# Performance work log

Measured on AMD Instinct MI355X. Metric: run time of the kernel, lower is better.

## Reference

```python
import jax, jax.numpy as jnp
import numpy as np

EPS = 1e-5

def _ln(z, g, b):
    # LayerNorm over last axis (per the gammas/betas of shape (2, 3H))
    mu = jnp.mean(z, axis=-1, keepdims=True)
    var = jnp.var(z, axis=-1, keepdims=True)
    return g * (z - mu) * jax.lax.rsqrt(var + EPS) + b

def setup_inputs() -> dict:
    key = jax.random.key(0)
    ks = jax.random.split(key, 12)
    B, L, D_IN, H, A, DEPTH = 64, 512, 256, 256, 128, 4
    glorot = lambda k, sh: jax.random.normal(k, sh, jnp.float32) * np.sqrt(2.0 / (sh[0] + sh[1])).astype(np.float32)
    # variable-length prefix masks (bucketing/masking semantics of the layer)
    lengths = jax.random.randint(ks[0], (B, 1), L // 2, L + 1)
    mask = jnp.arange(L)[None, :] < lengths
    return {
        'x': jax.random.normal(ks[1], (B, L, D_IN), jnp.float32),
        'mask': mask,
        'W_emb': glorot(ks[2], (D_IN, H)),
        'b_emb': jnp.zeros((H,), jnp.float32),
        'W': glorot(ks[3], (H, 3 * H)),
        'U': glorot(ks[4], (H, 3 * H)),
        'b': jnp.zeros((3 * H,), jnp.float32),
        'W_action_1': glorot(ks[5], (H, A)),
        'U_action_1': glorot(ks[6], (H, A)),
        'b_action_1': jnp.zeros((A,), jnp.float32),
        'W_action_2': glorot(ks[7], (A, 2)),
        'b_action_2': jnp.zeros((2,), jnp.float32),
        'gammas': jnp.ones((2, 3 * H), jnp.float32),
        'betas': jnp.zeros((2, 3 * H), jnp.float32),
        'depth': DEPTH,
    }

def _run_depth(x_seq, m_seq, W, U, b, Wa1, Ua1, ba1, Wa2, ba2, gammas, betas):
    # x_seq: (L,B,H), m_seq: (L,B) bool
    H = W.shape[0]
    B = x_seq.shape[1]
    # precompute + layernorm the input projection for all steps (fusable)
    xp_all = _ln(jnp.einsum('lbh,hk->lbk', x_seq, W), gammas[0], betas[0])  # (L,B,3H)

    def step(h, inputs):
        xp, xt, mt = inputs  # (B,3H), (B,H), (B,)
        hp = _ln(h @ U, gammas[1], betas[1])
        r = jax.nn.sigmoid(xp[:, :H] + hp[:, :H] + b[:H])
        z = jax.nn.sigmoid(xp[:, H:2 * H] + hp[:, H:2 * H] + b[H:2 * H])
        hh = jnp.tanh(xp[:, 2 * H:] + r * hp[:, 2 * H:] + b[2 * H:])
        h_new = z * h + (1.0 - z) * hh
        # action-policy subnetwork (binary merge/propagate decision)
        logits = jnp.tanh(xt @ Wa1 + h @ Ua1 + ba1) @ Wa2 + ba2  # (B,2)
        pol = jax.nn.softmax(logits, axis=-1)
        act = (pol[:, 1] > pol[:, 0]) & mt
        h_out = jnp.where(mt[:, None], h_new, h)  # masked steps carry state
        return h_out, (h_out, act, pol)

    h0 = jnp.zeros((B, H), x_seq.dtype)
    _, (h_seq, act_seq, pol_seq) = jax.lax.scan(step, h0, (xp_all, x_seq, m_seq))
    return h_seq, act_seq, pol_seq

def reference(x, mask, W_emb, b_emb, W, U, b, W_action_1, U_action_1, b_action_1,
              W_action_2, b_action_2, gammas, betas, depth):
    # embedding projection, then time-major like the Theano scans
    h_seq = jnp.swapaxes(x @ W_emb + b_emb, 0, 1)  # (L,B,H)
    m_seq = jnp.swapaxes(mask, 0, 1)               # (L,B)
    actions, policies = [], []
    for _ in range(depth):  # vertical (tree-depth) scan: small fixed count
        h_new, act, pol = _run_depth(h_seq, m_seq, W, U, b,
                                     W_action_1, U_action_1, b_action_1,
                                     W_action_2, b_action_2, gammas, betas)
        actions.append(act)
        policies.append(pol)
        h_seq = h_new
        m_seq = m_seq & act  # tree collapse: only selected nodes survive upward
    output = h_seq[-1]  # (B,H) final hidden state of top layer
    action = jnp.stack(actions, 0).transpose(2, 0, 1)      # (B,depth,L)
    policy = jnp.stack(policies, 0).transpose(2, 0, 1, 3)  # (B,depth,L,2)
    return output, action, policy
```

## Files before the change

### kernel.cpp

```cpp
#include <hip/hip_runtime.h>
#include <hip/hip_bf16.h>
#include <math.h>

#define BB 64
#define LL 512
#define HH 256
#define H3 768
#define AA 128
#define NDEPTH 4
#define NROWS (LL*BB)

#define EXCH_U64_PER_CHAIN (2 * 3 * 256)

typedef float vf32x32 __attribute__((ext_vector_type(32)));

#define HIDX(c) (36 * ((c) >> 5) + ((c) & 31))
#define HPAD 284

#define UVAL(f) ((f) < 32 ? u0v[(f)] : (f) < 64 ? u1v[(f)-32] \
                : (f) < 96 ? u2v[(f)-64] : u3v[(f)-96])

__global__ void maskcvt_kernel(const unsigned char* __restrict__ raw,
                               int* __restrict__ m)
{
    int i = blockIdx.x * blockDim.x + threadIdx.x;
    bool bytemode = (raw[1] == 1);
    int v;
    if (bytemode) v = raw[i] ? 1 : 0;
    else          v = (((const int*)raw)[i] != 0) ? 1 : 0;
    m[i] = v;
}

__global__ __launch_bounds__(512) void mkidx_kernel(
    const int* __restrict__ m,
    int* __restrict__ rowidx,
    int* __restrict__ nact)
{
    const int b    = blockIdx.x;
    const int tid  = threadIdx.x;
    const int lane = tid & 63;
    const int w    = tid >> 6;
    __shared__ int wcnt[8];
    int pred = m[b * LL + tid];
    unsigned long long bal = __ballot(pred != 0);
    int below = __popcll(bal & ((1ull << lane) - 1ull));
    if (lane == 63) wcnt[w] = __popcll(bal);
    __syncthreads();
    int woff = 0;
#pragma unroll
    for (int i = 0; i < 8; ++i) woff += (i < w) ? wcnt[i] : 0;
    if (pred) rowidx[b * LL + woff + below] = tid;
    if (tid == 511) nact[b] = woff + wcnt[7];
}

template<int MODE, int EPI>
__global__ __launch_bounds__(256) void gemm_kernel(
    const float* __restrict__ A, const float* __restrict__ Bm,
    const float* __restrict__ bias,
    float* __restrict__ C, int M, int N,
    const int* __restrict__ ridx, const int* __restrict__ nact)
{
    __shared__ float As[16][132];
    __shared__ float Bs[16][132];
    const int tid = threadIdx.x;
    const int tx = tid & 15, ty = tid >> 4;
    const int row0 = blockIdx.y * 128, col0 = blockIdx.x * 128;

    int arow0 = 0, arow1 = 0;
    if (MODE == 3) {
        const int bb = row0 >> 9;
        const int na = nact[bb];
        if ((row0 & 511) >= na) return;
        const int r0 = row0 + (tid >> 2);
        const int r1 = r0 + 64;
        const int l0 = ((r0 & 511) < na) ? ridx[r0] : 0;
        const int l1 = ((r1 & 511) < na) ? ridx[r1] : 0;
        arow0 = l0 * 64 + bb;
        arow1 = l1 * 64 + bb;
    }

    float acc[8][8];
#pragma unroll
    for (int i = 0; i < 8; ++i)
#pragma unroll
        for (int j = 0; j < 8; ++j) acc[i][j] = 0.f;

    for (int kk = 0; kk < 256; kk += 16) {
#pragma unroll
        for (int i = 0; i < 2; ++i) {
            int aid = i * 256 + tid;
            int r   = aid >> 2;
            int k4  = (aid & 3) << 2;
            int rr  = row0 + r;
            float4 v;
            if (MODE == 1) {
                v = *(const float4*)(A + (rr & 63) * 131072 + (rr >> 6) * 256 + kk + k4);
            } else {
                int ar = i ? arow1 : arow0;
                v = *(const float4*)(A + ar * 256 + kk + k4);
            }
            As[k4 + 0][r] = v.x; As[k4 + 1][r] = v.y;
            As[k4 + 2][r] = v.z; As[k4 + 3][r] = v.w;

            int bid = i * 256 + tid;
            int bk  = bid >> 5;
            int c4  = (bid & 31) << 2;
            float4 w = *(const float4*)(Bm + (kk + bk) * N + col0 + c4);
            *(float4*)&Bs[bk][c4] = w;
        }
        __syncthreads();
#pragma unroll
        for (int k = 0; k < 16; ++k) {
            float a[8], bb2[8];
            *(float4*)&a[0]   = *(const float4*)&As[k][ty * 8];
            *(float4*)&a[4]   = *(const float4*)&As[k][ty * 8 + 4];
            *(float4*)&bb2[0] = *(const float4*)&Bs[k][tx * 4];
            *(float4*)&bb2[4] = *(const float4*)&Bs[k][64 + tx * 4];
#pragma unroll
            for (int i = 0; i < 8; ++i)
#pragma unroll
                for (int j = 0; j < 8; ++j)
                    acc[i][j] += a[i] * bb2[j];
        }
        __syncthreads();
    }

#pragma unroll
    for (int i = 0; i < 8; ++i) {
        int row   = row0 + ty * 8 + i;
        int colb0 = col0 + tx * 4;
        int colb1 = col0 + 64 + tx * 4;
        float v0[4], v1[4];
#pragma unroll
        for (int j = 0; j < 4; ++j) {
            float a0 = acc[i][j], a1 = acc[i][4 + j];
            if (EPI == 1) { a0 += bias[colb0 + j]; a1 += bias[colb1 + j]; }
            v0[j] = a0; v1[j] = a1;
        }
        *(float4*)&C[row * N + colb0] = *(float4*)&v0[0];
        *(float4*)&C[row * N + colb1] = *(float4*)&v1[0];
    }
}

__global__ __launch_bounds__(256) void lnrows_kernel(
    float* __restrict__ XP, const float* __restrict__ g0,
    const float* __restrict__ b0, const float* __restrict__ gb,
    const int* __restrict__ nact)
{
    const int row = blockIdx.x;
    if ((row & 511) >= nact[row >> 9]) return;
    const int tid = threadIdx.x;
    float* p = XP + (long)row * H3;
    float v0 = p[tid], v1 = p[tid + 256], v2 = p[tid + 512];
    float s = v0 + v1 + v2;
    float q = v0 * v0 + v1 * v1 + v2 * v2;
#pragma unroll
    for (int off = 32; off >= 1; off >>= 1) {
        s += __shfl_xor(s, off);
        q += __shfl_xor(q, off);
    }
    __shared__ float rs4[4], rq4[4];
    if ((tid & 63) == 0) { rs4[tid >> 6] = s; rq4[tid >> 6] = q; }
    __syncthreads();
    float S = rs4[0] + rs4[1] + rs4[2] + rs4[3];
    float Q = rq4[0] + rq4[1] + rq4[2] + rq4[3];
    float mu  = S * (1.f / 768.f);
    float var = Q * (1.f / 768.f) - mu * mu;
    float r   = rsqrtf(var + 1e-5f);
    p[tid]       = g0[tid]       * (v0 - mu) * r + b0[tid]       + gb[tid];
    p[tid + 256] = g0[tid + 256] * (v1 - mu) * r + b0[tid + 256] + gb[tid + 256];
    p[tid + 512] = g0[tid + 512] * (v2 - mu) * r + b0[tid + 512] + gb[tid + 512];
}

__global__ __launch_bounds__(512, 2) void scan3_kernel(
    const float* __restrict__ XP,
    const float* __restrict__ U,
    const float* __restrict__ g1, const float* __restrict__ b1,
    const int* __restrict__ mask,
    float* __restrict__ Y,
    unsigned long long* __restrict__ exch,
    int seq0,
    const float* __restrict__ Xc,
    const float* __restrict__ Wa1,
    const float* __restrict__ ba1,
    float* __restrict__ XA)
{
    __shared__ float h_pad[HPAD];
    __shared__ float vrow[256];
    __shared__ float xp_lds[768];
    __shared__ float g1s[768], b1s[768];
    __shared__ int   mk[512];
    __shared__ float reds[4], redq[4];
    __shared__ float As[16][132];
    __shared__ float Bs[16][132];

    const int tid = threadIdx.x;

    if (blockIdx.x >= 192) {
        const int t    = blockIdx.x - 192;
        const int row0 = t * 128;
        const int tx   = tid & 15;
        const int ty4  = tid >> 4;
        float xacc[4][8];
#pragma unroll
        for (int i = 0; i < 4; ++i)
#pragma unroll
            for (int j = 0; j < 8; ++j) xacc[i][j] = 0.f;

        for (int kk = 0; kk < 256; kk += 16) {
            {
                int r  = tid >> 2;
                int k4 = (tid & 3) << 2;
                float4 v = *(const float4*)(Xc + (row0 + r) * 256 + kk + k4);
                As[k4 + 0][r] = v.x; As[k4 + 1][r] = v.y;
                As[k4 + 2][r] = v.z; As[k4 + 3][r] = v.w;
            }
            {
                int bk = tid >> 5;
                int c4 = (tid & 31) << 2;
                float4 w = *(const float4*)(Wa1 + (kk + bk) * AA + c4);
                *(float4*)&Bs[bk][c4] = w;
            }
            __syncthreads();
#pragma unroll
            for (int k = 0; k < 16; ++k) {
                float a[4], bb2[8];
                *(float4*)&a[0]   = *(const float4*)&As[k][ty4 * 4];
                *(float4*)&bb2[0] = *(const float4*)&Bs[k][tx * 4];
                *(float4*)&bb2[4] = *(const float4*)&Bs[k][64 + tx * 4];
#pragma unroll
                for (int i = 0; i < 4; ++i)
#pragma unroll
                    for (int j = 0; j < 8; ++j)
                        xacc[i][j] += a[i] * bb2[j];
            }
            __syncthreads();
        }
#pragma unroll
        for (int i = 0; i < 4; ++i) {
            int row = row0 + ty4 * 4 + i;
            float v0[4], v1[4];
#pragma unroll
            for (int j = 0; j < 4; ++j) {
                v0[j] = xacc[i][j]     + ba1[tx * 4 + j];
                v1[j] = xacc[i][4 + j] + ba1[64 + tx * 4 + j];
            }
            *(float4*)&XA[row * AA + tx * 4]      = *(float4*)&v0[0];
            *(float4*)&XA[row * AA + 64 + tx * 4] = *(float4*)&v1[0];
        }
        return;
    }

    const int i0   = blockIdx.x;
    const int xcd  = i0 & 7;
    const int slot = i0 >> 3;
    const int b    = xcd + 8 * (slot / 3);
    const int s    = slot % 3;
    const int kg   = tid & 7;
    const int cp   = tid >> 3;
    const int q1   = (s + 1 >= 3) ? s - 2 : s + 1;
    const int q2   = (s + 2 >= 3) ? s - 1 : s + 2;

    vf32x32 u0v, u1v, u2v, u3v;
    {
        const volatile float* Uv = U;
        const int colbase = s * 256 + 4 * cp;
#pragma unroll
        for (int i = 0; i < 8; ++i) {
#pragma unroll
            for (int t = 0; t < 16; ++t) {
                const int e = t >> 2, cj = t & 3;
                const int f = i * 16 + t;
                float val = Uv[(32 * kg + 4 * i + e) * H3 + colbase + cj];
                if      (f < 32) u0v[f]      = val;
                else if (f < 64) u1v[f - 32] = val;
                else if (f < 96) u2v[f - 64] = val;
                else             u3v[f - 96] = val;
            }
        }
    }
    for (int i = tid; i < HPAD; i += 512) h_pad[i] = 0.f;
    for (int i = tid; i < 768; i += 512) { g1s[i] = g1[i]; b1s[i] = b1[i]; }
    mk[tid] = mask[b * LL + tid];
    __syncthreads();

    unsigned long long* exb = exch + b * EXCH_U64_PER_CHAIN;
    int seq = seq0;

    for (int l = 0; l < LL; ++l) {
        if (!mk[l]) {
            if (s == 0 && tid < 64) {
                float4 hv = *(const float4*)&h_pad[HIDX(tid * 4)];
                *(float4*)&Y[((long)l * BB + b) * HH + tid * 4] = hv;
            }
            continue;
        }
        seq++;
        const int par = seq & 1;
        const int cs  = seq - seq0 - 1;

        float4 xr4;
        if (tid < 192) xr4 = *(const float4*)(XP + ((long)(b * LL + cs)) * H3 + tid * 4);

        float a0 = 0.f, a1 = 0.f, a2 = 0.f, a3 = 0.f;
#pragma unroll
        for (int i = 0; i < 8; ++i) {
            const float4 hv = *(const float4*)&h_pad[36 * kg + 4 * i];
#pragma unroll
            for (int e = 0; e < 4; ++e) {
                const float hh = (e == 0) ? hv.x : (e == 1) ? hv.y
                               : (e == 2) ? hv.z : hv.w;
                const int fb = i * 16 + e * 4;
                a0 += UVAL(fb + 0) * hh;
                a1 += UVAL(fb + 1) * hh;
                a2 += UVAL(fb + 2) * hh;
                a3 += UVAL(fb + 3) * hh;
            }
        }
#pragma unroll
        for (int off = 1; off < 8; off <<= 1) {
            a0 += __shfl_xor(a0, off);
            a1 += __shfl_xor(a1, off);
            a2 += __shfl_xor(a2, off);
            a3 += __shfl_xor(a3, off);
        }

        if (kg < 2) {
            const int c0 = 4 * cp + 2 * kg;
            const float pv0 = (kg == 0) ? a0 : a2;
            const float pv1 = (kg == 0) ? a1 : a3;
            unsigned long long pk0 =
                ((unsigned long long)(unsigned)seq << 32) |
                (unsigned long long)__float_as_uint(pv0);
            unsigned long long pk1 =
                ((unsigned long long)(unsigned)seq << 32) |
                (unsigned long long)__float_as_uint(pv1);
            __hip_atomic_store(&exb[(par * 3 + s) * 256 + c0], pk0,
                               __ATOMIC_RELAXED, __HIP_MEMORY_SCOPE_AGENT);
            __hip_atomic_store(&exb[(par * 3 + s) * 256 + c0 + 1], pk1,
                               __ATOMIC_RELAXED, __HIP_MEMORY_SCOPE_AGENT);
        } else if (kg == 2) {
            vrow[4 * cp]     = a0;
            vrow[4 * cp + 1] = a1;
        } else if (kg == 3) {
            vrow[4 * cp + 2] = a2;
            vrow[4 * cp + 3] = a3;
        }
        __syncthreads();

        if (tid < 192) *(float4*)&xp_lds[tid * 4] = xr4;

        float pre = 0.f, v0 = 0.f, v1 = 0.f, v2 = 0.f;
        if (tid < 256) {
            pre = vrow[tid];

            unsigned long long x1 = 0, x2 = 0;
            bool d1 = false, d2 = false;
            int spins = 0;
            do {
                unsigned long long t1 =
                    __hip_atomic_load(&exb[(par * 3 + q1) * 256 + tid],
                                      __ATOMIC_RELAXED, __HIP_MEMORY_SCOPE_AGENT);
                unsigned long long t2 =
                    __hip_atomic_load(&exb[(par * 3 + q2) * 256 + tid],
                                      __ATOMIC_RELAXED, __HIP_MEMORY_SCOPE_AGENT);
                if (!d1 && (int)(t1 >> 32) == seq) { x1 = t1; d1 = true; }
                if (!d2 && (int)(t2 >> 32) == seq) { x2 = t2; d2 = true; }
                if (++spins > 8) __builtin_amdgcn_s_sleep(1);
            } while (!(d1 && d2));
            float w1 = __uint_as_float((unsigned)x1);
            float w2 = __uint_as_float((unsigned)x2);
            v0 = (s == 0) ? pre : ((q1 == 0) ? w1 : w2);
            v1 = (s == 1) ? pre : ((q1 == 1) ? w1 : w2);
            v2 = (s == 2) ? pre : ((q1 == 2) ? w1 : w2);

            float st = v0 + v1 + v2;
            float qt = v0 * v0 + v1 * v1 + v2 * v2;
#pragma unroll
            for (int off = 32; off >= 1; off >>= 1) {
                st += __shfl_xor(st, off);
                qt += __shfl_xor(qt, off);
            }
            if ((tid & 63) == 0) { reds[tid >> 6] = st; redq[tid >> 6] = qt; }
        }
        __syncthreads();

        if (tid < 256) {
            float S = reds[0] + reds[1] + reds[2] + reds[3];
            float Q = redq[0] + redq[1] + redq[2] + redq[3];
            float mu = S * (1.f / 768.f);
            float rs = rsqrtf(Q * (1.f / 768.f) - mu * mu + 1e-5f);
            float hp_r = g1s[tid]       * (v0 - mu) * rs + b1s[tid];
            float hp_z = g1s[256 + tid] * (v1 - mu) * rs + b1s[256 + tid];
            float hp_h = g1s[512 + tid] * (v2 - mu) * rs + b1s[512 + tid];
            float xr = xp_lds[tid], xz = xp_lds[256 + tid], xh = xp_lds[512 + tid];
            float r  = 1.f / (1.f + expf(-(xr + hp_r)));
            float z  = 1.f / (1.f + expf(-(xz + hp_z)));
            float hh = tanhf(xh + r * hp_h);
            float o  = z * h_pad[HIDX(tid)] + (1.f - z) * hh;
            h_pad[HIDX(tid)] = o;
            if (s == 0) Y[((long)l * BB + b) * HH + tid] = o;
        }
        __syncthreads();
    }
}

__global__ __launch_bounds__(256) void gemmact_kernel(
    const float* __restrict__ Yprev,
    const float* __restrict__ Ua1,
    const float* __restrict__ XA,
    const float* __restrict__ Wa2,
    const float* __restrict__ ba2,
    const int* __restrict__ mask_in, int* __restrict__ mask_out,
    float* __restrict__ act_out, float* __restrict__ pol_out, int d)
{
    __shared__ float As[16][132];
    __shared__ float Bs[16][132];
    const int tid = threadIdx.x;
    const int tx = tid & 15, ty = tid >> 4;
    const int row0 = blockIdx.y * 128;

    float acc[8][8];
#pragma unroll
    for (int i = 0; i < 8; ++i)
#pragma unroll
        for (int j = 0; j < 8; ++j) acc[i][j] = 0.f;

    for (int kk = 0; kk < 256; kk += 16) {
#pragma unroll
        for (int i = 0; i < 2; ++i) {
            int aid = i * 256 + tid;
            int r   = aid >> 2;
            int k4  = (aid & 3) << 2;
            int rr  = row0 + r;
            float4 v;
            if (rr < 64) v = make_float4(0.f, 0.f, 0.f, 0.f);
            else         v = *(const float4*)(Yprev + (rr - 64) * 256 + kk + k4);
            As[k4 + 0][r] = v.x; As[k4 + 1][r] = v.y;
            As[k4 + 2][r] = v.z; As[k4 + 3][r] = v.w;

            int bid = i * 256 + tid;
            int bk  = bid >> 5;
            int c4  = (bid & 31) << 2;
            float4 w = *(const float4*)(Ua1 + (kk + bk) * AA + c4);
            *(float4*)&Bs[bk][c4] = w;
        }
        __syncthreads();
#pragma unroll
        for (int k = 0; k < 16; ++k) {
            float a[8], bb2[8];
            *(float4*)&a[0]   = *(const float4*)&As[k][ty * 8];
            *(float4*)&a[4]   = *(const float4*)&As[k][ty * 8 + 4];
            *(float4*)&bb2[0] = *(const float4*)&Bs[k][tx * 4];
            *(float4*)&bb2[4] = *(const float4*)&Bs[k][64 + tx * 4];
#pragma unroll
            for (int i = 0; i < 8; ++i)
#pragma unroll
                for (int j = 0; j < 8; ++j)
                    acc[i][j] += a[i] * bb2[j];
        }
        __syncthreads();
    }

    float p0[8], p1[8];
#pragma unroll
    for (int i = 0; i < 8; ++i) { p0[i] = 0.f; p1[i] = 0.f; }
#pragma unroll
    for (int i = 0; i < 8; ++i) {
        int row = row0 + ty * 8 + i;
#pragma unroll
        for (int j = 0; j < 8; ++j) {
            int c   = (j < 4) ? (tx * 4 + j) : (64 + tx * 4 + (j - 4));
            float v = tanhf(acc[i][j] + XA[row * AA + c]);
            p0[i] += v * Wa2[c * 2];
            p1[i] += v * Wa2[c * 2 + 1];
        }
    }
#pragma unroll
    for (int off = 1; off < 16; off <<= 1) {
#pragma unroll
        for (int i = 0; i < 8; ++i) {
            p0[i] += __shfl_xor(p0[i], off);
            p1[i] += __shfl_xor(p1[i], off);
        }
    }
    if (tx == 0) {
#pragma unroll
        for (int i = 0; i < 8; ++i) {
            int row = row0 + ty * 8 + i;
            int l   = row >> 6, bb = row & 63;
            float l0 = p0[i] + ba2[0];
            float l1 = p1[i] + ba2[1];
            float m  = fmaxf(l0, l1);
            float e0 = expf(l0 - m), e1 = expf(l1 - m);
            float inv = 1.f / (e0 + e1);
            float q0 = e0 * inv, q1v = e1 * inv;
            int mt = mask_in[bb * LL + l];
            int a  = (q1v > q0) && mt;
            act_out[bb * (NDEPTH * LL) + d * LL + l] = a ? 1.f : 0.f;
            pol_out[bb * (NDEPTH * LL * 2) + d * (LL * 2) + l * 2 + 0] = q0;
            pol_out[bb * (NDEPTH * LL * 2) + d * (LL * 2) + l * 2 + 1] = q1v;
            mask_out[bb * LL + l] = a;
        }
    }
}

__global__ void final_copy_kernel(const float* __restrict__ X, float* __restrict__ out)
{
    int i = blockIdx.x * blockDim.x + threadIdx.x;
    int bb = i >> 8, j = i & 255;
    out[i] = X[((long)(LL - 1) * BB + bb) * HH + j];
}

extern "C" void kernel_launch(void* const* d_in, const int* in_sizes, int n_in,
                              void* d_out, int out_size, void* d_ws, size_t ws_size,
                              hipStream_t stream)
{
    const float* x      = (const float*)d_in[0];
    const void*  mraw   = d_in[1];
    const float* W_emb  = (const float*)d_in[2];
    const float* b_emb  = (const float*)d_in[3];
    const float* W      = (const float*)d_in[4];
    const float* U      = (const float*)d_in[5];
    const float* bias3  = (const float*)d_in[6];
    const float* Wa1    = (const float*)d_in[7];
    const float* Ua1    = (const float*)d_in[8];
    const float* ba1    = (const float*)d_in[9];
    const float* Wa2    = (const float*)d_in[10];
    const float* ba2    = (const float*)d_in[11];
    const float* gammas = (const float*)d_in[12];
    const float* betas  = (const float*)d_in[13];

    float* out = (float*)d_out;
    char*  ws  = (char*)d_ws;

    float* XP = (float*)(ws);
    float* X  = (float*)(ws + 100663296UL);
    float* Y  = (float*)(ws + 134217728UL);
    float* XA = (float*)(ws + 167772160UL);
    int*   m0 = (int*)(ws + 184549376UL);
    int*   m1 = (int*)(ws + 184680448UL);
    unsigned long long* exch_d = (unsigned long long*)(ws + 184811520UL);

    float* act_out = out + BB * HH;
    float* pol_out = act_out + BB * NDEPTH * LL;

    maskcvt_kernel<<<dim3(NROWS / 256), dim3(256), 0, stream>>>(
        (const unsigned char*)mraw, m0);

    gemm_kernel<1, 1><<<dim3(2, 256), dim3(256), 0, stream>>>(
        x, W_emb, b_emb, X, NROWS, HH, nullptr, nullptr);

    float* Xc = X; float* Yc = Y;
    int* mc = m0; int* mn = m1;

    for (int d = 0; d < NDEPTH; ++d) {
        int* rowidx = (int*)Yc;
        int* nactp  = ((int*)Yc) + NROWS;

        mkidx_kernel<<<dim3(BB), dim3(512), 0, stream>>>(mc, rowidx, nactp);

        gemm_kernel<3, 0><<<dim3(6, 256), dim3(256), 0, stream>>>(
            Xc, W, nullptr, XP, NROWS, H3, rowidx, nactp);
        lnrows_kernel<<<dim3(NROWS), dim3(256), 0, stream>>>(
            XP, gammas, betas, bias3, nactp);

        scan3_kernel<<<dim3(448), dim3(512), 0, stream>>>(
            XP, U, gammas + H3, betas + H3, mc, Yc, exch_d, d << 10,
            Xc, Wa1, ba1, XA);

        gemmact_kernel<<<dim3(1, 256), dim3(256), 0, stream>>>(
            Yc, Ua1, XA, Wa2, ba2, mc, mn, act_out, pol_out, d);

        { float* tmp = Xc; Xc = Yc; Yc = tmp; }
        { int* tmp = mc; mc = mn; mn = tmp; }
    }

    final_copy_kernel<<<dim3(BB), dim3(256), 0, stream>>>(Xc, out);
}
```

Baseline: 3.275 ms.

## Exchange per-slice LayerNorm partial sums across blocks to drop a barrier

Each block computes the sum and sum-of-squares of its own 256-column slice of h@U before the exchange and publishes them in two extra slots of the inter-block exchange buffer. Consumers then poll for those two partials alongside the row values. The final LayerNorm statistics come from three partial sums, so the block-wide reduction and one __syncthreads per timestep are gone from the serial recurrence. The cost is four more atomic loads per spin iteration and a padded exchange slice layout. Summing partials in a different order can change floating-point rounding slightly.

```diff
diff --git a/kernel.cpp b/kernel.cpp
--- a/kernel.cpp
+++ b/kernel.cpp
@@ -10,7 +10,8 @@
 #define NDEPTH 4
 #define NROWS (LL*BB)
 
-#define EXCH_U64_PER_CHAIN (2 * 3 * 256)
+#define EXCH_SLICE_U64 264
+#define EXCH_U64_PER_CHAIN (2 * 3 * EXCH_SLICE_U64)
 
 typedef float vf32x32 __attribute__((ext_vector_type(32)));
 
@@ -190,7 +191,7 @@
     __shared__ float xp_lds[768];
     __shared__ float g1s[768], b1s[768];
     __shared__ int   mk[512];
-    __shared__ float reds[4], redq[4];
+    __shared__ float swS[8], swQ[8];
     __shared__ float As[16][132];
     __shared__ float Bs[16][132];
 
@@ -335,9 +336,9 @@
             unsigned long long pk1 =
                 ((unsigned long long)(unsigned)seq << 32) |
                 (unsigned long long)__float_as_uint(pv1);
-            __hip_atomic_store(&exb[(par * 3 + s) * 256 + c0], pk0,
+            __hip_atomic_store(&exb[(par * 3 + s) * EXCH_SLICE_U64 + c0], pk0,
                                __ATOMIC_RELAXED, __HIP_MEMORY_SCOPE_AGENT);
-            __hip_atomic_store(&exb[(par * 3 + s) * 256 + c0 + 1], pk1,
+            __hip_atomic_store(&exb[(par * 3 + s) * EXCH_SLICE_U64 + c0 + 1], pk1,
                                __ATOMIC_RELAXED, __HIP_MEMORY_SCOPE_AGENT);
         } else if (kg == 2) {
             vrow[4 * cp]     = a0;
@@ -346,48 +347,76 @@
             vrow[4 * cp + 2] = a2;
             vrow[4 * cp + 3] = a3;
         }
+
+        {
+            float ts = a0 + a1 + a2 + a3;
+            float tq = a0 * a0 + a1 * a1 + a2 * a2 + a3 * a3;
+#pragma unroll
+            for (int off = 8; off < 64; off <<= 1) {
+                ts += __shfl_xor(ts, off);
+                tq += __shfl_xor(tq, off);
+            }
+            if ((tid & 63) == 0) { swS[tid >> 6] = ts; swQ[tid >> 6] = tq; }
+        }
         __syncthreads();
 
+        if (tid < 2) {
+            float* sw = (tid == 0) ? swS : swQ;
+            float acc8 = sw[0] + sw[1] + sw[2] + sw[3]
+                       + sw[4] + sw[5] + sw[6] + sw[7];
+            unsigned long long pks =
+                ((unsigned long long)(unsigned)seq << 32) |
+                (unsigned long long)__float_as_uint(acc8);
+            __hip_atomic_store(&exb[(par * 3 + s) * EXCH_SLICE_U64 + 256 + tid],
+                               pks, __ATOMIC_RELAXED, __HIP_MEMORY_SCOPE_AGENT);
+        }
         if (tid < 192) *(float4*)&xp_lds[tid * 4] = xr4;
 
-        float pre = 0.f, v0 = 0.f, v1 = 0.f, v2 = 0.f;
         if (tid < 256) {
-            pre = vrow[tid];
-
-            unsigned long long x1 = 0, x2 = 0;
-            bool d1 = false, d2 = false;
-            int spins = 0;
+            const float pre = vrow[tid];
+            float Sl = swS[0] + swS[1] + swS[2] + swS[3]
+                     + swS[4] + swS[5] + swS[6] + swS[7];
+            float Ql = swQ[0] + swQ[1] + swQ[2] + swQ[3]
+                     + swQ[4] + swQ[5] + swQ[6] + swQ[7];
+
+            const int e1v = (par * 3 + q1) * EXCH_SLICE_U64 + tid;
+            const int e2v = (par * 3 + q2) * EXCH_SLICE_U64 + tid;
+            const int e1s = (par * 3 + q1) * EXCH_SLICE_U64 + 256;
+            const int e2s = (par * 3 + q2) * EXCH_SLICE_U64 + 256;
+            unsigned long long xv1 = 0, xv2 = 0, xs1 = 0, xq1 = 0, xs2 = 0, xq2 = 0;
+            int done = 0, spins = 0;
             do {
-                unsigned long long t1 =
-                    __hip_atomic_load(&exb[(par * 3 + q1) * 256 + tid],
-                                      __ATOMIC_RELAXED, __HIP_MEMORY_SCOPE_AGENT);
-                unsigned long long t2 =
-                    __hip_atomic_load(&exb[(par * 3 + q2) * 256 + tid],
-                                      __ATOMIC_RELAXED, __HIP_MEMORY_SCOPE_AGENT);
-                if (!d1 && (int)(t1 >> 32) == seq) { x1 = t1; d1 = true; }
-                if (!d2 && (int)(t2 >> 32) == seq) { x2 = t2; d2 = true; }
+                unsigned long long t1 = __hip_atomic_load(&exb[e1v],
+                    __ATOMIC_RELAXED, __HIP_MEMORY_SCOPE_AGENT);
+                unsigned long long t2 = __hip_atomic_load(&exb[e2v],
+                    __ATOMIC_RELAXED, __HIP_MEMORY_SCOPE_AGENT);
+                unsigned long long u1 = __hip_atomic_load(&exb[e1s],
+                    __ATOMIC_RELAXED, __HIP_MEMORY_SCOPE_AGENT);
+                unsigned long long u2 = __hip_atomic_load(&exb[e1s + 1],
+                    __ATOMIC_RELAXED, __HIP_MEMORY_SCOPE_AGENT);
+                unsigned long long u3 = __hip_atomic_load(&exb[e2s],
+                    __ATOMIC_RELAXED, __HIP_MEMORY_SCOPE_AGENT);
+                unsigned long long u4 = __hip_atomic_load(&exb[e2s + 1],
+                    __ATOMIC_RELAXED, __HIP_MEMORY_SCOPE_AGENT);
+                if (!(done & 1)  && (int)(t1 >> 32) == seq) { xv1 = t1; done |= 1; }
+                if (!(done & 2)  && (int)(t2 >> 32) == seq) { xv2 = t2; done |= 2; }
+                if (!(done & 4)  && (int)(u1 >> 32) == seq) { xs1 = u1; done |= 4; }
+                if (!(done & 8)  && (int)(u2 >> 32) == seq) { xq1 = u2; done |= 8; }
+                if (!(done & 16) && (int)(u3 >> 32) == seq) { xs2 = u3; done |= 16; }
+                if (!(done & 32) && (int)(u4 >> 32) == seq) { xq2 = u4; done |= 32; }
                 if (++spins > 8) __builtin_amdgcn_s_sleep(1);
-            } while (!(d1 && d2));
-            float w1 = __uint_as_float((unsigned)x1);
-            float w2 = __uint_as_float((unsigned)x2);
-            v0 = (s == 0) ? pre : ((q1 == 0) ? w1 : w2);
-            v1 = (s == 1) ? pre : ((q1 == 1) ? w1 : w2);
-            v2 = (s == 2) ? pre : ((q1 == 2) ? w1 : w2);
-
-            float st = v0 + v1 + v2;
-            float qt = v0 * v0 + v1 * v1 + v2 * v2;
-#pragma unroll
-            for (int off = 32; off >= 1; off >>= 1) {
-                st += __shfl_xor(st, off);
-                qt += __shfl_xor(qt, off);
-            }
-            if ((tid & 63) == 0) { reds[tid >> 6] = st; redq[tid >> 6] = qt; }
-        }
-        __syncthreads();
-
-        if (tid < 256) {
-            float S = reds[0] + reds[1] + reds[2] + reds[3];
-            float Q = redq[0] + redq[1] + redq[2] + redq[3];
+            } while (done != 63);
+
+            float w1 = __uint_as_float((unsigned)xv1);
+            float w2 = __uint_as_float((unsigned)xv2);
+            float v0 = (s == 0) ? pre : ((q1 == 0) ? w1 : w2);
+            float v1 = (s == 1) ? pre : ((q1 == 1) ? w1 : w2);
+            float v2 = (s == 2) ? pre : ((q1 == 2) ? w1 : w2);
+            float S  = Sl + __uint_as_float((unsigned)xs1)
+                          + __uint_as_float((unsigned)xs2);
+            float Q  = Ql + __uint_as_float((unsigned)xq1)
+                          + __uint_as_float((unsigned)xq2);
+
             float mu = S * (1.f / 768.f);
             float rs = rsqrtf(Q * (1.f / 768.f) - mu * mu + 1e-5f);
             float hp_r = g1s[tid]       * (v0 - mu) * rs + b1s[tid];
```

Result: slower. 3.424 ms (+4.5%).
